# Kernel tuning notes

Hardware: AMD Instinct MI355X
Metric: run time of the kernel (lower is better)

## Reference

```python
import jax, jax.numpy as jnp
import numpy as np

LMBDA = 100.0
GAMMA = 0.5  # resolvant_gamma


def setup_inputs() -> dict:
    key = jax.random.key(0)
    ks = jax.random.split(key, 8)
    B, Vx, Vy, C, K = 1, 5000, 5000, 128, 64
    feat_x = jax.random.normal(ks[0], (B, Vx, C), dtype=jnp.float32)
    feat_y = jax.random.normal(ks[1], (B, Vy, C), dtype=jnp.float32)
    # positive, sorted eigenvalues (Laplacian spectrum)
    evals_x = jnp.sort(jax.random.uniform(ks[2], (B, K), minval=0.01, maxval=10.0), axis=-1)
    evals_y = jnp.sort(jax.random.uniform(ks[3], (B, K), minval=0.01, maxval=10.0), axis=-1)
    # pseudo-inverse eigenvector rows, scaled ~1/sqrt(V) for realistic magnitudes
    evecs_trans_x = jax.random.normal(ks[4], (B, K, Vx), dtype=jnp.float32) / np.sqrt(Vx)
    evecs_trans_y = jax.random.normal(ks[5], (B, K, Vy), dtype=jnp.float32) / np.sqrt(Vy)
    # sqrt mass matrices: well-conditioned near-identity (must be invertible)
    eye = jnp.eye(K, dtype=jnp.float32)
    sqrtMk_x = eye[None] + 0.05 * jax.random.normal(ks[6], (B, K, K), dtype=jnp.float32)
    sqrtMk_y = eye[None] + 0.05 * jax.random.normal(ks[7], (B, K, K), dtype=jnp.float32)
    return {
        "feat_x": feat_x, "feat_y": feat_y,
        "evals_x": evals_x, "evals_y": evals_y,
        "evecs_trans_x": evecs_trans_x, "evecs_trans_y": evecs_trans_y,
        "sqrtMk_x": sqrtMk_x, "sqrtMk_y": sqrtMk_y,
    }


def _compute_fmap(fx, fy, ex, ey, Px, Py, Mx, My):
    # fx:[V,C] fy:[V,C] ex,ey:[K] Px,Py:[K,V] Mx,My:[K,K]
    A = Px @ fx                 # [K,C] spectral coeffs of source feats
    Bc = My @ (Py @ fy)         # adapt_feature=True: [K,C]
    k, m = A.shape
    vec_B = Bc.T.reshape(m * k, 1)
    # Ik = sqrtMk_y (adapt_feature, no dev_feature)
    At_Ik = jnp.kron(A.T, My)   # [m*k, k*k]
    first = At_Ik.T @ At_Ik     # [k*k, k*k]
    # adapt_mask=True branch: resolvent mask as Kronecker operators
    inv_Mx = jnp.linalg.inv(Mx)
    s = jnp.maximum(jnp.max(ex), jnp.max(ey))
    g1 = (ex / s) ** GAMMA
    g2 = (ey / s) ** GAMMA
    rn1_re = g1 / (g1 * g1 + 1.0)
    rn1_im = 1.0 / (g1 * g1 + 1.0)
    rn2_re = g2 / (g2 * g2 + 1.0)
    rn2_im = 1.0 / (g2 * g2 + 1.0)
    lx_re = jnp.kron(rn1_re[:, None] * inv_Mx, My)          # diag(rn1_re)@inv_Mx
    lx_im = jnp.kron(rn1_im[:, None] * inv_Mx, My)
    ly_re = jnp.kron(inv_Mx, My * rn2_re[None, :])          # My@diag(rn2_re)
    ly_im = jnp.kron(inv_Mx, My * rn2_im[None, :])
    D_re = ly_re - lx_re
    D_im = ly_im - lx_im
    second = D_re.T @ D_re + D_im.T @ D_im
    rhs = At_Ik.T @ vec_B
    op = first + LMBDA * second
    C = jnp.linalg.solve(op, rhs).reshape(k, k).T
    return C[None]  # [1,K,K]


def reference(feat_x, feat_y, evals_x, evals_y, evecs_trans_x, evecs_trans_y, sqrtMk_x, sqrtMk_y):
    Cxy = _compute_fmap(
        feat_x[0], feat_y[0], evals_x[0], evals_y[0],
        evecs_trans_x[0], evecs_trans_y[0], sqrtMk_x[0], sqrtMk_y[0],
    )
    return Cxy  # bidirectional=False -> Cyx is None
```

## Files before the change

kernel.cpp:

```cpp
#include <hip/hip_runtime.h>

#define NV 5000
#define LMB 100.0f
#define MAXIT 150
#define TOL 1e-10f
#define NBLK 32
#define NALL 96
#define BSZ 512

#define SV_O     0
#define CTRL_O   256
#define PART_O   2048
#define AH_O     657408
#define B0_O     665600
#define H_O      673792
#define E_O      677888
#define Z2_O     681984
#define ZH_O     686080
#define Q0_O     690176
#define LIH_O    702464
#define LIE_O    706560
#define U0_O     710656
#define LH_O     747520
#define BT_O     751616
#define RSTK_O   755712
#define LCT_O    772096
#define WG_O     788480
#define XG_O     792576
#define WS_NEED  796672

#define MS_O     PART_O
#define PRT2_O   (PART_O + 16384)
#define ZERO_N   35712

#define LCTS_S   0
#define RPK_S    12288
#define TPART_S  12800
#define TPACK_S  15920
#define SPART_S  16304
#define SM_FLOATS 21504

typedef unsigned long long u64;
union PKu { u64 u; float2 f; };

__device__ __forceinline__ float aload(const float* p) {
  return __hip_atomic_load(p, __ATOMIC_RELAXED, __HIP_MEMORY_SCOPE_AGENT);
}
__device__ __forceinline__ void astore(float* p, float v) {
  __hip_atomic_store(p, v, __ATOMIC_RELAXED, __HIP_MEMORY_SCOPE_AGENT);
}
__device__ __forceinline__ u64 aload64(const u64* p) {
  return __hip_atomic_load(p, __ATOMIC_RELAXED, __HIP_MEMORY_SCOPE_AGENT);
}
__device__ __forceinline__ void astore64(u64* p, u64 v) {
  __hip_atomic_store(p, v, __ATOMIC_RELAXED, __HIP_MEMORY_SCOPE_AGENT);
}

__device__ __forceinline__ void gbar(int* cb, int phase, int blk, int per) {
  __syncthreads();
  if (threadIdx.x == 0)
    __hip_atomic_fetch_add(cb + phase * 128 + (blk & 7) * 16, 1,
                           __ATOMIC_ACQ_REL, __HIP_MEMORY_SCOPE_AGENT);
  if (threadIdx.x < 64) {
    for (;;) {
      int v = (threadIdx.x < 8)
        ? __hip_atomic_load(cb + phase * 128 + threadIdx.x * 16,
                            __ATOMIC_ACQUIRE, __HIP_MEMORY_SCOPE_AGENT)
        : per;
      if (__all(v >= per)) break;
      __builtin_amdgcn_s_sleep(2);
    }
  }
  __syncthreads();
}

__device__ __forceinline__ void stageN(float* dst, const float* src) {
  for (int e = threadIdx.x; e < 4096; e += BSZ)
    dst[(e >> 6) * 65 + (e & 63)] = src[e];
}
__device__ __forceinline__ void stageT(float* dst, const float* src) {
  for (int e = threadIdx.x; e < 4096; e += BSZ)
    dst[(e & 63) * 65 + (e >> 6)] = src[e];
}
__device__ __forceinline__ void mm65(const float* Ls, const float* Rs, float* D) {
  for (int e = threadIdx.x; e < 4096; e += BSZ) {
    int i = e >> 6, j = e & 63;
    float a0 = 0.f, a1 = 0.f;
#pragma unroll 8
    for (int t = 0; t < 64; t += 2) {
      a0 = fmaf(Ls[i * 65 + t], Rs[t * 65 + j], a0);
      a1 = fmaf(Ls[i * 65 + t + 1], Rs[(t + 1) * 65 + j], a1);
    }
    D[e] = a0 + a1;
  }
}
__device__ __forceinline__ void mm65L(const float* Ls, const float* Rs, float* DL) {
  for (int e = threadIdx.x; e < 4096; e += BSZ) {
    int i = e >> 6, j = e & 63;
    float a0 = 0.f, a1 = 0.f;
#pragma unroll 8
    for (int t = 0; t < 64; t += 2) {
      a0 = fmaf(Ls[i * 65 + t], Rs[t * 65 + j], a0);
      a1 = fmaf(Ls[i * 65 + t + 1], Rs[(t + 1) * 65 + j], a1);
    }
    DL[i * 65 + j] = a0 + a1;
  }
}
__device__ void mmNN_s(const float* L, const float* R, float* D, float* sm) {
  stageN(sm, L); stageN(sm + 4160, R);
  __syncthreads();
  mm65(sm, sm + 4160, D);
}

__device__ void chol_inv(const float* S, float* Li, float* Lf, float* sm) {
  float (*M)[65] = (float (*)[65])sm;
  float (*T)[65] = (float (*)[65])(sm + 64 * 65);
  int tid = threadIdx.x;
  for (int e = tid; e < 4096; e += BSZ) {
    M[e >> 6][e & 63] = S[e];
    T[e >> 6][e & 63] = 0.f;
  }
  __syncthreads();
  for (int j = 0; j < 64; ++j) {
    if (tid < 63 - j) M[j + 1 + tid][j] *= rsqrtf(M[j][j]);
    __syncthreads();
    int m = 63 - j, c2 = (m * (m + 1)) >> 1;
    for (int e = tid; e < c2; e += BSZ) {
      int rp = (int)((sqrtf(8.f * (float)e + 1.f) - 1.f) * 0.5f);
      while (((rp + 1) * (rp + 2)) >> 1 <= e) ++rp;
      while ((rp * (rp + 1)) >> 1 > e) --rp;
      int cp = e - ((rp * (rp + 1)) >> 1);
      int r = j + 1 + rp, c = j + 1 + cp;
      M[r][c] = fmaf(-M[r][j], M[c][j], M[r][c]);
    }
    __syncthreads();
  }
  if (tid < 64) {
    int c = tid;
    T[c][c] = rsqrtf(M[c][c]);
    for (int r = c + 1; r < 64; ++r) {
      float s = 0.f;
      for (int t = c; t < r; ++t) s = fmaf(M[r][t], T[t][c], s);
      T[r][c] = -s * rsqrtf(M[r][r]);
    }
  }
  __syncthreads();
  if (Lf) {
    for (int e = tid; e < 4096; e += BSZ) {
      int r = e >> 6, c = e & 63;
      Lf[e] = (r > c) ? M[r][c] : ((r == c) ? sqrtf(M[r][c]) : 0.f);
    }
  }
  for (int e = tid; e < 4096; e += BSZ) Li[e] = T[e >> 6][e & 63];
}

__device__ __forceinline__ float coop_apply(float* sm, const float* yv, float y_own,
                                            int lane, int wv8) {
  const float* LCTs = sm + LCTS_S;
  const float* Rpk = sm + RPK_S;
  float* Tpart = sm + TPART_S;
  float* Tpack = sm + TPACK_S;
  float* Spart = sm + SPART_S;
  float t1p[6];
#pragma unroll
  for (int p = 0; p < 6; ++p) t1p[p] = 0.f;
#pragma unroll
  for (int u = 0; u < 8; ++u) {
    int m = u * 8 + wv8;
    float yu = yv[u];
    float4 rA = *(const float4*)&Rpk[m * 8 + 0];
    float2 rB = *(const float2*)&Rpk[m * 8 + 4];
    t1p[0] = fmaf(yu, rA.x, t1p[0]);  t1p[1] = fmaf(yu, rA.y, t1p[1]);
    t1p[2] = fmaf(yu, rA.z, t1p[2]);  t1p[3] = fmaf(yu, rA.w, t1p[3]);
    t1p[4] = fmaf(yu, rB.x, t1p[4]);  t1p[5] = fmaf(yu, rB.y, t1p[5]);
  }
#pragma unroll
  for (int p = 0; p < 6; ++p) Tpart[wv8 * 390 + p * 65 + lane] = t1p[p];
  __syncthreads();
  int tid = wv8 * 64 + lane;
  if (tid < 384) {
    int tk = tid >> 1, c = tid & 1;
    int p = (tk >> 6) * 2 + c, k = tk & 63;
    Tpack[tid] = (((Tpart[0 * 390 + p * 65 + k] + Tpart[1 * 390 + p * 65 + k]) +
                   (Tpart[2 * 390 + p * 65 + k] + Tpart[3 * 390 + p * 65 + k])) +
                  ((Tpart[4 * 390 + p * 65 + k] + Tpart[5 * 390 + p * 65 + k]) +
                   (Tpart[6 * 390 + p * 65 + k] + Tpart[7 * 390 + p * 65 + k])));
  }
  __syncthreads();
  float s0 = 0.f, s1 = 0.f;
  int tk0 = wv8 * 24;
#pragma unroll 8
  for (int q = 0; q < 24; ++q) {
    int tk = tk0 + q;
    float lv = LCTs[tk * 64 + lane];
    float2 tv = *(const float2*)&Tpack[tk * 2];
    s0 = fmaf(lv, tv.x, s0);
    s1 = fmaf(lv, tv.y, s1);
  }
  Spart[wv8 * 128 + 0 * 64 + lane] = s0;
  Spart[wv8 * 128 + 1 * 64 + lane] = s1;
  __syncthreads();
  int cw = (wv8 & 1) * 64 + lane;
  return y_own + (((Spart[0 * 128 + cw] + Spart[1 * 128 + cw]) +
                   (Spart[2 * 128 + cw] + Spart[3 * 128 + cw])) +
                  ((Spart[4 * 128 + cw] + Spart[5 * 128 + cw]) +
                   (Spart[6 * 128 + cw] + Spart[7 * 128 + cw])));
}

__global__ __launch_bounds__(BSZ) void solve_kernel(const float* fx, const float* fy,
                                                    const float* ex, const float* ey,
                                                    const float* Px, const float* Py,
                                                    const float* Mx, const float* My,
                                                    float* W, float* out) {
  __shared__ float sm[SM_FLOATS] __attribute__((aligned(16)));
  __shared__ float sLd[192], sRd[192], wred[4], scal[2];
  int tid = threadIdx.x, blk = blockIdx.x;
  int* cb = (int*)(W + CTRL_O);

  if (blk < 80) {
    int mat = (blk >= 40), seg = mat ? (blk - 40) : blk;
    const float* P = (mat ? Py : Px);
    const float* f = (mat ? fy : fx);
    int v0 = seg * 125;
    for (int e = tid; e < 8000; e += BSZ) {
      int rr = e / 125, vv = e - rr * 125;
      sm[rr * 126 + vv] = P[rr * NV + v0 + vv];
    }
    __syncthreads();
    int rg = (tid >> 5) << 2;
    int cq = (tid & 31) << 2;
    float acc[4][4];
#pragma unroll
    for (int u = 0; u < 4; ++u)
#pragma unroll
      for (int v = 0; v < 4; ++v) acc[u][v] = 0.f;
    for (int v5 = 0; v5 < 125; v5 += 5) {
      float4 fv[5];
#pragma unroll
      for (int q = 0; q < 5; ++q)
        fv[q] = *(const float4*)(f + (size_t)(v0 + v5 + q) * 128 + cq);
#pragma unroll
      for (int q = 0; q < 5; ++q) {
#pragma unroll
        for (int u = 0; u < 4; ++u) {
          float pv = sm[(rg + u) * 126 + v5 + q];
          acc[u][0] = fmaf(pv, fv[q].x, acc[u][0]);
          acc[u][1] = fmaf(pv, fv[q].y, acc[u][1]);
          acc[u][2] = fmaf(pv, fv[q].z, acc[u][2]);
          acc[u][3] = fmaf(pv, fv[q].w, acc[u][3]);
        }
      }
    }
    float* O = W + PART_O + (size_t)blk * 8192;
#pragma unroll
    for (int u = 0; u < 4; ++u) {
      float4 o = make_float4(acc[u][0], acc[u][1], acc[u][2], acc[u][3]);
      *(float4*)(O + (rg + u) * 128 + cq) = o;
    }
  } else if (blk < 82) {
    for (int e = tid; e < 4096; e += BSZ) sm[(e >> 6) * 65 + (e & 63)] = My[e];
    __syncthreads();
    int base = (blk - 80) * 2048;
    for (int e = tid; e < 2048; e += BSZ) {
      int i = (base + e) >> 6, j = (base + e) & 63;
      float a0 = 0.f, a1 = 0.f;
#pragma unroll 8
      for (int t = 0; t < 64; t += 2) {
        a0 = fmaf(sm[t * 65 + i], sm[t * 65 + j], a0);
        a1 = fmaf(sm[(t + 1) * 65 + i], sm[(t + 1) * 65 + j], a1);
      }
      W[H_O + base + e] = a0 + a1;
    }
  } else if (blk == 82) {
    if (tid < 64) {
      float vx = ex[tid], vy = ey[tid];
      float m = fmaxf(vx, vy);
#pragma unroll
      for (int o = 32; o > 0; o >>= 1) m = fmaxf(m, __shfl_xor(m, o, 64));
      float g1 = sqrtf(vx / m), g2 = sqrtf(vy / m);
      float d1 = 1.f / fmaf(g1, g1, 1.f), d2 = 1.f / fmaf(g2, g2, 1.f);
      W[SV_O + tid] = g1 * d1;
      W[SV_O + 64 + tid] = d1;
      W[SV_O + 128 + tid] = g2 * d2;
      W[SV_O + 192 + tid] = d2;
    }
  }
  gbar(cb, 0, blk, 12);
  if (blk >= NBLK) return;

  if (blk == 0) {
    chol_inv(W + H_O, W + LIH_O, W + LH_O, sm);
  } else if (blk <= 19) {
    int item = blk;
    if (item <= 8) {
      int c0 = (item - 1) * 16;
      float* ssum = sm;
      float* mxs = sm + 1088;
      for (int e = tid; e < 4096; e += BSZ) mxs[(e >> 6) * 65 + (e & 63)] = Mx[e];
      for (int e = tid; e < 1024; e += BSZ) {
        int t = e >> 4, cl = e & 15;
        float s = 0.f;
        for (int p = 0; p < 40; ++p) s += W[PART_O + (size_t)p * 8192 + t * 128 + c0 + cl];
        ssum[t * 17 + cl] = s;
      }
      __syncthreads();
      for (int e = tid; e < 1024; e += BSZ) {
        int i = e >> 4, cl = e & 15;
        float a0 = 0.f, a1 = 0.f;
#pragma unroll 8
        for (int t = 0; t < 64; t += 2) {
          a0 = fmaf(mxs[t * 65 + i], ssum[t * 17 + cl], a0);
          a1 = fmaf(mxs[(t + 1) * 65 + i], ssum[(t + 1) * 17 + cl], a1);
        }
        W[AH_O + i * 128 + c0 + cl] = a0 + a1;
      }
    } else if (item <= 16) {
      int base = (item - 9) * 1024;
      for (int e = tid; e < 1024; e += BSZ) {
        float s = 0.f;
        for (int p = 0; p < 40; ++p) s += W[PART_O + (size_t)(40 + p) * 8192 + base + e];
        W[B0_O + base + e] = s;
      }
    } else {
      if (tid < 256) sm[tid] = W[SV_O + tid];
      __syncthreads();
      int t = item - 17;
      for (int e = tid; e < 4096; e += BSZ) {
        int k = e >> 6, b = e & 63;
        float h = W[H_O + e], v;
        if (t == 0) v = h * (sm[128 + k] * sm[128 + b] + sm[192 + k] * sm[192 + b]);
        else if (t == 1) v = h * (sm[128 + k] + sm[128 + b]);
        else v = h * (sm[192 + k] + sm[192 + b]);
        W[Q0_O + t * 4096 + e] = v;
      }
    }
  }
  gbar(cb, 1, blk, 4);

  if (blk < 4) {
    for (int e = tid; e < 8192; e += BSZ) {
      int i = e >> 7, c = e & 127;
      sm[c * 65 + i] = W[AH_O + e];
    }
    __syncthreads();
    int i0 = blk * 16;
    for (int e = tid; e < 1024; e += BSZ) {
      int i = i0 + (e >> 6), j = e & 63;
      float a0 = 0.f, a1 = 0.f;
#pragma unroll 8
      for (int c = 0; c < 128; c += 2) {
        a0 = fmaf(sm[c * 65 + i], sm[c * 65 + j], a0);
        a1 = fmaf(sm[(c + 1) * 65 + i], sm[(c + 1) * 65 + j], a1);
      }
      float acc = a0 + a1;
      if (i == j) {
        float a = W[SV_O + i], b = W[SV_O + 64 + i];
        acc += LMB * (a * a + b * b);
      }
      W[E_O + i * 64 + j] = acc;
    }
  } else if (blk < 8) {
    int i0 = (blk - 4) * 16;
    for (int e = tid; e < 8192; e += BSZ) {
      int j = e >> 7, c = e & 127;
      sm[c * 65 + j] = W[B0_O + e];
    }
    for (int e = tid; e < 2048; e += BSZ) {
      int il = e >> 7, c = e & 127;
      sm[8320 + c * 17 + il] = W[AH_O + (i0 + il) * 128 + c];
    }
    __syncthreads();
    for (int e = tid; e < 1024; e += BSZ) {
      int il = e >> 6, j = e & 63;
      float a0 = 0.f, a1 = 0.f;
#pragma unroll 8
      for (int c = 0; c < 128; c += 2) {
        a0 = fmaf(sm[8320 + c * 17 + il], sm[c * 65 + j], a0);
        a1 = fmaf(sm[8320 + (c + 1) * 17 + il], sm[(c + 1) * 65 + j], a1);
      }
      W[Z2_O + (i0 + il) * 64 + j] = a0 + a1;
    }
  } else if (blk < 11) {
    int t = blk - 8;
    mmNN_s(W + LIH_O, W + Q0_O + t * 4096, W + U0_O + t * 4096, sm);
  } else {
    for (int e = (blk - 11) * BSZ + tid; e < ZERO_N; e += 21 * BSZ)
      W[MS_O + e] = 0.f;
  }
  gbar(cb, 2, blk, 4);

  if (blk == 0) chol_inv(W + E_O, W + LIE_O, nullptr, sm);
  else if (blk == 1) mmNN_s(W + Z2_O, W + LH_O, W + ZH_O, sm);
  else if (blk < 5) {
    int t = blk - 2;
    stageN(sm, W + U0_O + t * 4096);
    stageT(sm + 4160, W + LIH_O);
    __syncthreads();
    mm65L(sm, sm + 4160, sm + 8320);
    __syncthreads();
    for (int e = tid; e < 4096; e += BSZ) {
      int a = e >> 6, b = e & 63;
      W[RSTK_O + t * 4096 + e] = 0.5f * (sm[8320 + a * 65 + b] + sm[8320 + b * 65 + a]);
    }
  }
  gbar(cb, 3, blk, 4);

  if (blk == 0) mmNN_s(W + LIE_O, W + ZH_O, W + BT_O, sm);
  else if (blk == 1) {
    stageN(sm, W + LIE_O);
    stageT(sm + 4160, W + LIE_O);
    __syncthreads();
    mm65L(sm, sm + 4160, sm + 8320);
    __syncthreads();
    for (int e = tid; e < 4096; e += BSZ) {
      int k = e >> 6, i = e & 63;
      W[LCT_O + e] = LMB * 0.5f * (sm[8320 + k * 65 + i] + sm[8320 + i * 65 + k]);
    }
  } else if (blk < 4) {
    float* dv = sLd;
    if (tid < 64) dv[tid] = W[SV_O + ((blk == 2) ? tid : 64 + tid)];
    stageN(sm, W + LIE_O);
    __syncthreads();
    for (int e = tid; e < 4096; e += BSZ) {
      int jq = e >> 6, k = e & 63;
      sm[4160 + k * 65 + jq] = sm[jq * 65 + k] * dv[k];
    }
    __syncthreads();
    mm65L(sm, sm + 4160, sm + 8320);
    __syncthreads();
    int t = blk - 1;
    for (int e = tid; e < 4096; e += BSZ) {
      int k = e >> 6, i = e & 63;
      W[LCT_O + t * 4096 + e] = -LMB * 0.5f * (sm[8320 + k * 65 + i] + sm[8320 + i * 65 + k]);
    }
  }
  gbar(cb, 4, blk, 4);

  int lane = tid & 63, wv8 = tid >> 6;
  int jown = blk * 2 + wv8;
  const float* BTp = W + BT_O;
  const float* LCTp = W + LCT_O;
  const float* RSTKp = W + RSTK_O;
  u64* MS = (u64*)(W + MS_O);
  u64* PR2 = (u64*)(W + PRT2_O);
  const float* LCTs = sm + LCTS_S;
  const float* Rpk = sm + RPK_S;
  float* Tpart = sm + TPART_S;
  float* Tpack = sm + TPACK_S;
  float* Spart = sm + SPART_S;

  for (int e = tid; e < 12288; e += BSZ) sm[LCTS_S + e] = LCTp[e];
  if (tid < 384) {
    int m = tid / 6, p = tid - m * 6;
    int t = p >> 1, c = p & 1;
    sm[RPK_S + m * 8 + p] = RSTKp[(t * 64 + blk * 2 + c) * 64 + m];
  }
  if (tid < 192) {
    int t = tid >> 6, i = tid & 63;
    sLd[tid] = LCTp[t * 4096 + i * 64 + i];
    sRd[tid] = RSTKp[t * 4096 + i * 64 + i];
  }
  __syncthreads();
  float yv0[8];
#pragma unroll
  for (int u = 0; u < 8; ++u) {
    int col = u * 8 + wv8;
    float den = 1.f + sLd[lane] * sRd[col] + sLd[64 + lane] * sRd[64 + col] +
                sLd[128 + lane] * sRd[128 + col];
    yv0[u] = BTp[lane * 64 + col] / den;
  }
  float invd = 0.f, u_l = 0.f, r_l = 0.f, m_l = 0.f;
  if (wv8 < 2) {
    invd = 1.f / (1.f + sLd[lane] * sRd[jown] + sLd[64 + lane] * sRd[64 + jown] +
                  sLd[128 + lane] * sRd[128 + jown]);
    u_l = BTp[lane * 64 + jown] * invd;
    r_l = BTp[lane * 64 + jown];
  }
  float w_l = coop_apply(sm, yv0, u_l, lane, wv8);
  if (wv8 < 2) {
    m_l = invd * w_l;
    PKu pk; pk.f = make_float2(m_l, 1.f);
    astore64(MS + jown * 64 + lane, pk.u);
    float vr = r_l * u_l, vw = w_l * u_l;
#pragma unroll
    for (int o = 32; o; o >>= 1) { vr += __shfl_down(vr, o, 64); vw += __shfl_down(vw, o, 64); }
    if (lane == 0) { wred[wv8 * 2] = vr; wred[wv8 * 2 + 1] = vw; }
  }
  __syncthreads();
  if (tid == 0) {
    PKu a, b;
    a.f = make_float2(wred[0] + wred[2], 1.f);
    b.f = make_float2(wred[1] + wred[3], 1.f);
    astore64(PR2 + (size_t)blk * 2, a.u);
    astore64(PR2 + (size_t)blk * 2 + 1, b.u);
  }

  float p_l = 0.f, q_l = 0.f, z_l = 0.f, s_l = 0.f, x_l = 0.f;
  float gprev = 1.f, aprev = 1.f, g0b = 1.f;
  int sl = lane & 31;
  for (int j = 0; j < MAXIT; ++j) {
    unsigned sbits = __float_as_uint((float)(j + 1));
    const u64* msrc = MS + (size_t)(j & 1) * 4096;
    const u64* ps = PR2 + ((size_t)j * 32 + sl) * 2;
    u64 ra = 0, rb = 0;
    if (wv8 == 0) { ra = aload64(ps); rb = aload64(ps + 1); }
    float t1p[6];
#pragma unroll
    for (int p = 0; p < 6; ++p) t1p[p] = 0.f;
    u64 raw8[8];
#pragma unroll
    for (int u = 0; u < 8; ++u) raw8[u] = aload64(msrc + u * BSZ + tid);
    unsigned done = 0;
    int spins = 0;
    while (done != 0xFFu) {
#pragma unroll
      for (int u = 0; u < 8; ++u) {
        if (!((done >> u) & 1u)) {
          u64 v = raw8[u];
          if ((unsigned)(v >> 32) == sbits) {
            float yu = __uint_as_float((unsigned)v);
            int m = u * 8 + wv8;
            float4 rA = *(const float4*)&Rpk[m * 8 + 0];
            float2 rB = *(const float2*)&Rpk[m * 8 + 4];
            t1p[0] = fmaf(yu, rA.x, t1p[0]);
            t1p[1] = fmaf(yu, rA.y, t1p[1]);
            t1p[2] = fmaf(yu, rA.z, t1p[2]);
            t1p[3] = fmaf(yu, rA.w, t1p[3]);
            t1p[4] = fmaf(yu, rB.x, t1p[4]);
            t1p[5] = fmaf(yu, rB.y, t1p[5]);
            done |= (1u << u);
          } else {
            raw8[u] = aload64(msrc + u * BSZ + tid);
          }
        }
      }
      if (done != 0xFFu && ++spins > 64) {
        __hip_atomic_load(msrc + tid, __ATOMIC_ACQUIRE, __HIP_MEMORY_SCOPE_AGENT);
        spins = 0;
      }
    }
#pragma unroll
    for (int p = 0; p < 6; ++p) Tpart[wv8 * 390 + p * 65 + lane] = t1p[p];
    __syncthreads();
    if (wv8 >= 2) {
      int z = tid - 128;
      int tk = z >> 1, c = z & 1;
      int p = (tk >> 6) * 2 + c, k = tk & 63;
      Tpack[z] = (((Tpart[0 * 390 + p * 65 + k] + Tpart[1 * 390 + p * 65 + k]) +
                   (Tpart[2 * 390 + p * 65 + k] + Tpart[3 * 390 + p * 65 + k])) +
                  ((Tpart[4 * 390 + p * 65 + k] + Tpart[5 * 390 + p * 65 + k]) +
                   (Tpart[6 * 390 + p * 65 + k] + Tpart[7 * 390 + p * 65 + k])));
    } else if (wv8 == 0) {
      int spins2 = 0;
      for (;;) {
        bool ok = ((unsigned)(ra >> 32) == sbits) && ((unsigned)(rb >> 32) == sbits);
        if (__all(ok)) break;
        if (++spins2 > 64) {
          __hip_atomic_load(ps, __ATOMIC_ACQUIRE, __HIP_MEMORY_SCOPE_AGENT);
          spins2 = 0;
        }
        if ((unsigned)(ra >> 32) != sbits) ra = aload64(ps);
        if ((unsigned)(rb >> 32) != sbits) rb = aload64(ps + 1);
      }
      float pr = __uint_as_float((unsigned)ra), pw = __uint_as_float((unsigned)rb);
#pragma unroll
      for (int mm = 1; mm < 32; mm <<= 1) {
        pr += __shfl_xor(pr, mm, 64);
        pw += __shfl_xor(pw, mm, 64);
      }
      if (lane == 0) { scal[0] = pr; scal[1] = pw; }
    }
    __syncthreads();
    float gjb = scal[0], djb = scal[1];
    if (j == 0) g0b = gjb;
    if (j > 0 && fabsf(gjb) < TOL * fabsf(g0b)) break;
    float s0 = 0.f, s1 = 0.f;
    int tk0 = wv8 * 24;
#pragma unroll 8
    for (int q = 0; q < 24; ++q) {
      int tk = tk0 + q;
      float lv = LCTs[tk * 64 + lane];
      float2 tv = *(const float2*)&Tpack[tk * 2];
      s0 = fmaf(lv, tv.x, s0);
      s1 = fmaf(lv, tv.y, s1);
    }
    Spart[wv8 * 128 + 0 * 64 + lane] = s0;
    Spart[wv8 * 128 + 1 * 64 + lane] = s1;
    __syncthreads();
    if (wv8 < 2) {
      int cw = wv8 * 64 + lane;
      float n_l = m_l + (((Spart[0 * 128 + cw] + Spart[1 * 128 + cw]) +
                          (Spart[2 * 128 + cw] + Spart[3 * 128 + cw])) +
                         ((Spart[4 * 128 + cw] + Spart[5 * 128 + cw]) +
                          (Spart[6 * 128 + cw] + Spart[7 * 128 + cw])));
      float bj = (j == 0) ? 0.f : gjb / gprev;
      float aj = (j == 0) ? gjb / djb : gjb / (djb - bj * gjb / aprev);
      float z_n = fmaf(bj, z_l, n_l);
      float w_n = fmaf(-aj, z_n, w_l);
      float m_n = invd * w_n;
      PKu pk; pk.f = make_float2(m_n, (float)(j + 2));
      astore64(MS + (size_t)((j + 1) & 1) * 4096 + jown * 64 + lane, pk.u);
      q_l = fmaf(bj, q_l, m_l);
      s_l = fmaf(bj, s_l, w_l);
      p_l = fmaf(bj, p_l, u_l);
      x_l = fmaf(aj, p_l, x_l);
      r_l = fmaf(-aj, s_l, r_l);
      u_l = fmaf(-aj, q_l, u_l);
      z_l = z_n; w_l = w_n; m_l = m_n;
      float vr = r_l * u_l, vw = w_l * u_l;
#pragma unroll
      for (int o = 32; o; o >>= 1) { vr += __shfl_down(vr, o, 64); vw += __shfl_down(vw, o, 64); }
      if (lane == 0) { wred[wv8 * 2] = vr; wred[wv8 * 2 + 1] = vw; }
      gprev = gjb; aprev = aj;
    }
    __syncthreads();
    if (tid == 0) {
      PKu a, b;
      a.f = make_float2(wred[0] + wred[2], (float)(j + 2));
      b.f = make_float2(wred[1] + wred[3], (float)(j + 2));
      astore64(PR2 + ((size_t)(j + 1) * 32 + blk) * 2, a.u);
      astore64(PR2 + ((size_t)(j + 1) * 32 + blk) * 2 + 1, b.u);
    }
  }
  if (wv8 < 2) astore(W + XG_O + jown * 64 + lane, x_l);
  gbar(cb, 5, blk, 4);

  if (blk == 0) {
    float* Ys = sm;
    float* Ms2 = sm + 4160;
    for (int e = tid; e < 4096; e += BSZ) Ys[(e >> 6) * 65 + (e & 63)] = aload(W + XG_O + e);
    for (int e = tid; e < 4096; e += BSZ) Ms2[(e >> 6) * 65 + (e & 63)] = W[LIE_O + e];
    __syncthreads();
    for (int e = tid; e < 4096; e += BSZ) {
      int t = e >> 6, b = e & 63;
      float acc = 0.f;
#pragma unroll 8
      for (int a = 0; a < 64; ++a) acc = fmaf(Ms2[a * 65 + t], Ys[b * 65 + a], acc);
      W[WG_O + t * 64 + b] = acc;
    }
    __syncthreads();
    for (int e = tid; e < 4096; e += BSZ) Ys[(e >> 6) * 65 + (e & 63)] = W[WG_O + e];
    for (int e = tid; e < 4096; e += BSZ) Ms2[(e >> 6) * 65 + (e & 63)] = W[LIH_O + e];
    __syncthreads();
    for (int e = tid; e < 4096; e += BSZ) {
      int t = e >> 6, c = e & 63;
      float acc = 0.f;
#pragma unroll 8
      for (int b = 0; b < 64; ++b) acc = fmaf(Ys[t * 65 + b], Ms2[b * 65 + c], acc);
      W[WG_O + t * 64 + c] = acc;
    }
    __syncthreads();
    for (int e = tid; e < 4096; e += BSZ) Ys[(e >> 6) * 65 + (e & 63)] = W[WG_O + e];
    for (int e = tid; e < 4096; e += BSZ) Ms2[(e & 63) * 65 + (e >> 6)] = Mx[e];
    __syncthreads();
    for (int e = tid; e < 4096; e += BSZ) {
      int r = e >> 6, c = e & 63;
      float acc = 0.f;
#pragma unroll 8
      for (int t = 0; t < 64; ++t) acc = fmaf(Ms2[t * 65 + c], Ys[t * 65 + r], acc);
      out[e] = acc;
    }
  }
}

extern "C" void kernel_launch(void* const* d_in, const int* in_sizes, int n_in,
                              void* d_out, int out_size, void* d_ws, size_t ws_size,
                              hipStream_t stream) {
  const float* fx = (const float*)d_in[0];
  const float* fy = (const float*)d_in[1];
  const float* ex = (const float*)d_in[2];
  const float* ey = (const float*)d_in[3];
  const float* Px = (const float*)d_in[4];
  const float* Py = (const float*)d_in[5];
  const float* Mx = (const float*)d_in[6];
  const float* My = (const float*)d_in[7];
  float* out = (float*)d_out;
  float* W = (float*)d_ws;

  if (ws_size < (size_t)WS_NEED * sizeof(float)) {
    hipMemsetAsync(d_out, 0, (size_t)out_size * sizeof(float), stream);
    return;
  }

  hipMemsetAsync(W + CTRL_O, 0, 3072, stream);
  solve_kernel<<<NALL, BSZ, 0, stream>>>(fx, fy, ex, ey, Px, Py, Mx, My, W, out);
}
```

Before: 351.6 us.

## Publish per-wave CG partial dot products directly and add stagnation early exit

Each of the two active waves now writes its own reduced dot-product partial straight to global memory, tagged with the iteration number, instead of staging through shared memory behind a block barrier and a single-thread store. Consumers read 64 partials and reduce them with a full-wave shuffle. This removes one __syncthreads per CG iteration from the cross-block critical path. It also adds a patience-based stop: the loop exits when the residual has not dropped by 10% within 30 iterations. That can end iterations early but risks stopping before full convergence.

```diff
diff --git a/kernel.cpp b/kernel.cpp
--- a/kernel.cpp
+++ b/kernel.cpp
@@ -4,6 +4,7 @@
 #define LMB 100.0f
 #define MAXIT 150
 #define TOL 1e-10f
+#define PATIENCE 30
 #define NBLK 32
 #define NALL 96
 #define BSZ 512
@@ -31,7 +32,7 @@
 
 #define MS_O     PART_O
 #define PRT2_O   (PART_O + 16384)
-#define ZERO_N   35712
+#define ZERO_N   55040
 
 #define LCTS_S   0
 #define RPK_S    12288
@@ -213,7 +214,7 @@
                                                     const float* Mx, const float* My,
                                                     float* W, float* out) {
   __shared__ float sm[SM_FLOATS] __attribute__((aligned(16)));
-  __shared__ float sLd[192], sRd[192], wred[4], scal[2];
+  __shared__ float sLd[192], sRd[192], scal[2];
   int tid = threadIdx.x, blk = blockIdx.x;
   int* cb = (int*)(W + CTRL_O);
 
@@ -484,24 +485,23 @@
     float vr = r_l * u_l, vw = w_l * u_l;
 #pragma unroll
     for (int o = 32; o; o >>= 1) { vr += __shfl_down(vr, o, 64); vw += __shfl_down(vw, o, 64); }
-    if (lane == 0) { wred[wv8 * 2] = vr; wred[wv8 * 2 + 1] = vw; }
-  }
-  __syncthreads();
-  if (tid == 0) {
-    PKu a, b;
-    a.f = make_float2(wred[0] + wred[2], 1.f);
-    b.f = make_float2(wred[1] + wred[3], 1.f);
-    astore64(PR2 + (size_t)blk * 2, a.u);
-    astore64(PR2 + (size_t)blk * 2 + 1, b.u);
+    if (lane == 0) {
+      PKu a, b;
+      a.f = make_float2(vr, 1.f);
+      b.f = make_float2(vw, 1.f);
+      astore64(PR2 + (size_t)jown * 2, a.u);
+      astore64(PR2 + (size_t)jown * 2 + 1, b.u);
+    }
   }
 
   float p_l = 0.f, q_l = 0.f, z_l = 0.f, s_l = 0.f, x_l = 0.f;
   float gprev = 1.f, aprev = 1.f, g0b = 1.f;
-  int sl = lane & 31;
+  float gmin = 3.4e38f;
+  int lastimp = 0;
   for (int j = 0; j < MAXIT; ++j) {
     unsigned sbits = __float_as_uint((float)(j + 1));
     const u64* msrc = MS + (size_t)(j & 1) * 4096;
-    const u64* ps = PR2 + ((size_t)j * 32 + sl) * 2;
+    const u64* ps = PR2 + ((size_t)j * 64 + lane) * 2;
     u64 ra = 0, rb = 0;
     if (wv8 == 0) { ra = aload64(ps); rb = aload64(ps + 1); }
     float t1p[6];
@@ -564,7 +564,7 @@
       }
       float pr = __uint_as_float((unsigned)ra), pw = __uint_as_float((unsigned)rb);
 #pragma unroll
-      for (int mm = 1; mm < 32; mm <<= 1) {
+      for (int mm = 1; mm < 64; mm <<= 1) {
         pr += __shfl_xor(pr, mm, 64);
         pw += __shfl_xor(pw, mm, 64);
       }
@@ -573,7 +573,9 @@
     __syncthreads();
     float gjb = scal[0], djb = scal[1];
     if (j == 0) g0b = gjb;
-    if (j > 0 && fabsf(gjb) < TOL * fabsf(g0b)) break;
+    float agj = fabsf(gjb);
+    if (agj < 0.9f * gmin) { gmin = agj; lastimp = j; }
+    if (j > 0 && (agj < TOL * fabsf(g0b) || (j - lastimp) > PATIENCE)) break;
     float s0 = 0.f, s1 = 0.f;
     int tk0 = wv8 * 24;
 #pragma unroll 8
@@ -610,16 +612,14 @@
       float vr = r_l * u_l, vw = w_l * u_l;
 #pragma unroll
       for (int o = 32; o; o >>= 1) { vr += __shfl_down(vr, o, 64); vw += __shfl_down(vw, o, 64); }
-      if (lane == 0) { wred[wv8 * 2] = vr; wred[wv8 * 2 + 1] = vw; }
+      if (lane == 0) {
+        PKu a, b;
+        a.f = make_float2(vr, (float)(j + 2));
+        b.f = make_float2(vw, (float)(j + 2));
+        astore64(PR2 + ((size_t)(j + 1) * 64 + jown) * 2, a.u);
+        astore64(PR2 + ((size_t)(j + 1) * 64 + jown) * 2 + 1, b.u);
+      }
       gprev = gjb; aprev = aj;
-    }
-    __syncthreads();
-    if (tid == 0) {
-      PKu a, b;
-      a.f = make_float2(wred[0] + wred[2], (float)(j + 2));
-      b.f = make_float2(wred[1] + wred[3], (float)(j + 2));
-      astore64(PR2 + ((size_t)(j + 1) * 32 + blk) * 2, a.u);
-      astore64(PR2 + ((size_t)(j + 1) * 32 + blk) * 2 + 1, b.u);
     }
   }
   if (wv8 < 2) astore(W + XG_O + jown * 64 + lane, x_l);
```

Result: slower. 371.9 us (+5.7%).
